# Kernel optimization log

Measured on AMD Instinct MI355X. Metric: run time of the kernel, lower is better.

## Reference

```python
import jax, jax.numpy as jnp
import numpy as np

B, S, D, H, DFF = 4, 2048, 1024, 16, 4096
HD = D // H
EPS = 1e-12

def _layernorm(x, g, b):
    mu = jnp.mean(x, axis=-1, keepdims=True)
    var = jnp.mean(jnp.square(x - mu), axis=-1, keepdims=True)
    return (x - mu) * jax.lax.rsqrt(var + EPS) * g + b

def setup_inputs() -> dict:
    key = jax.random.key(0)
    ks = jax.random.split(key, 12)
    sd = 0.02
    inp = {
        'hidden_states': jax.random.normal(ks[0], (B, S, D), jnp.float32),
        'attention_mask': jnp.zeros((B, 1, 1, S), jnp.float32),
        'Wq': jax.random.normal(ks[1], (D, D), jnp.float32) * sd,
        'bq': jnp.zeros((D,), jnp.float32),
        'Wk': jax.random.normal(ks[2], (D, D), jnp.float32) * sd,
        'bk': jnp.zeros((D,), jnp.float32),
        'Wv': jax.random.normal(ks[3], (D, D), jnp.float32) * sd,
        'bv': jnp.zeros((D,), jnp.float32),
        'Wo': jax.random.normal(ks[4], (D, D), jnp.float32) * sd,
        'bo': jnp.zeros((D,), jnp.float32),
        'ln1_g': jnp.ones((D,), jnp.float32),
        'ln1_b': jnp.zeros((D,), jnp.float32),
        'Wi': jax.random.normal(ks[5], (D, DFF), jnp.float32) * sd,
        'bi': jnp.zeros((DFF,), jnp.float32),
        'Wo2': jax.random.normal(ks[6], (DFF, D), jnp.float32) * sd,
        'bo2': jnp.zeros((D,), jnp.float32),
        'ln2_g': jnp.ones((D,), jnp.float32),
        'ln2_b': jnp.zeros((D,), jnp.float32),
    }
    return inp

def reference(hidden_states, attention_mask, Wq, bq, Wk, bk, Wv, bv, Wo, bo,
              ln1_g, ln1_b, Wi, bi, Wo2, bo2, ln2_g, ln2_b):
    x = hidden_states  # [B,S,D]
    # project and split heads -> [B,H,S,hd]
    def heads(t):
        return t.reshape(B, S, H, HD).transpose(0, 2, 1, 3)
    q = heads(x @ Wq + bq)
    k = heads(x @ Wk + bk)
    v = heads(x @ Wv + bv)
    scores = jnp.einsum('bhqd,bhkd->bhqk', q, k) / np.float32(np.sqrt(HD))
    scores = scores + attention_mask  # additive mask broadcast [B,1,1,S]
    weights = jax.nn.softmax(scores, axis=-1)
    ctx = jnp.einsum('bhqk,bhkd->bhqd', weights, v)
    ctx = ctx.transpose(0, 2, 1, 3).reshape(B, S, D)
    attn_out = _layernorm(ctx @ Wo + bo + x, ln1_g, ln1_b)
    # FFN (gelu) with residual + LayerNorm
    h = jax.nn.gelu(attn_out @ Wi + bi, approximate=False)
    out = _layernorm(h @ Wo2 + bo2 + attn_out, ln2_g, ln2_b)
    return out
```

## Files before the change

### kernel.cpp

```cpp
#include <hip/hip_runtime.h>
#include <hip/hip_bf16.h>
#include <math.h>

#define B_   4
#define S_   2048
#define D_   1024
#define H_   16
#define HD_  64
#define DFF_ 4096
#define M_   (B_*S_)

typedef __bf16 bf16x8 __attribute__((ext_vector_type(8)));
typedef __bf16 bf16x4 __attribute__((ext_vector_type(4)));
typedef float  floatx4 __attribute__((ext_vector_type(4)));

__device__ __forceinline__ float  b2f(__bf16 v) { return (float)v; }
__device__ __forceinline__ __bf16 f2b(float v)  { return (__bf16)v; }

__device__ __forceinline__ void async_ld16(const void* g, void* l) {
    __builtin_amdgcn_global_load_lds(
        (const __attribute__((address_space(1))) unsigned int*)g,
        (__attribute__((address_space(3))) unsigned int*)l, 16, 0, 0);
}

__global__ void transpose_conv_kernel(const float* __restrict__ in,
                                      __bf16* __restrict__ out, int R, int C,
                                      float scale)
{
    __shared__ float t[32][33];
    int c0 = blockIdx.x * 32, r0 = blockIdx.y * 32;
    int tx = threadIdx.x, ty = threadIdx.y;
    for (int i = ty; i < 32; i += 8)
        t[i][tx] = in[(long)(r0 + i) * C + c0 + tx];
    __syncthreads();
    for (int i = ty; i < 32; i += 8)
        out[(long)(c0 + i) * R + r0 + tx] = f2b(t[tx][i] * scale);
}

__global__ void vt_transpose_kernel(const __bf16* __restrict__ qkv,
                                    __bf16* __restrict__ vtg)
{
    __shared__ __bf16 t[32][34];
    int b  = blockIdx.z;
    int h  = blockIdx.y >> 1;
    int d0 = (blockIdx.y & 1) * 32;
    int s0 = blockIdx.x * 32;
    int tx = threadIdx.x, ty = threadIdx.y;
    for (int i = ty; i < 32; i += 8)
        t[i][tx] = qkv[(long)(b * S_ + s0 + i) * 3072 + 2048 + h * 64 + d0 + tx];
    __syncthreads();
    for (int i = ty; i < 32; i += 8)
        vtg[((long)(b * H_ + h) * 64 + d0 + i) * S_ + s0 + tx] = t[tx][i];
}

__global__ void f2b_kernel(const float* __restrict__ in, __bf16* __restrict__ out,
                           long n)
{
    long i = ((long)blockIdx.x * 256 + threadIdx.x) * 8;
    if (i >= n) return;
    float4 a = *(const float4*)&in[i];
    float4 c = *(const float4*)&in[i + 4];
    union { __bf16 h[8]; uint4 u; } p;
    p.h[0] = f2b(a.x); p.h[1] = f2b(a.y); p.h[2] = f2b(a.z); p.h[3] = f2b(a.w);
    p.h[4] = f2b(c.x); p.h[5] = f2b(c.y); p.h[6] = f2b(c.z); p.h[7] = f2b(c.w);
    *(uint4*)&out[i] = p.u;
}

__global__ void bias_concat_kernel(const float* __restrict__ bq,
                                   const float* __restrict__ bk,
                                   const float* __restrict__ bv,
                                   float* __restrict__ dst)
{
    int i = blockIdx.x * 256 + threadIdx.x;
    if (i >= 3 * D_) return;
    float v = (i < D_) ? bq[i] * 0.125f
            : (i < 2 * D_) ? bk[i - D_] : bv[i - 2 * D_];
    dst[i] = v;
}

template<int MODE>
__global__ __launch_bounds__(256, 2)
void gemm_kernel(const __bf16* __restrict__ A, const __bf16* __restrict__ Bt,
                 const float* __restrict__ bias, const float* __restrict__ resid,
                 float* __restrict__ Cf, __bf16* __restrict__ Cb,
                 int M, int N, int K)
{
    __shared__ __bf16 sA[128 * 64];
    __shared__ __bf16 sB[128 * 64];

    const int tid  = threadIdx.x;
    const int lane = tid & 63;
    const int wave = tid >> 6;
    const int wm   = (wave >> 1) * 64;
    const int wn   = (wave & 1) * 64;
    const long bm  = (long)blockIdx.y * 128;
    const long bn  = (long)blockIdx.x * 128;

    floatx4 acc[4][4];
#pragma unroll
    for (int i = 0; i < 4; ++i)
#pragma unroll
        for (int j = 0; j < 4; ++j)
#pragma unroll
            for (int r = 0; r < 4; ++r) acc[i][j][r] = 0.0f;

    const int mrow = lane & 15;
    const int quad = lane >> 4;
    const int koff0 = ((0 * 4 + quad) ^ (mrow & 7)) * 8;
    const int koff1 = ((1 * 4 + quad) ^ (mrow & 7)) * 8;

    for (int k0 = 0; k0 < K; k0 += 64) {
        __syncthreads();
#pragma unroll
        for (int t = 0; t < 4; ++t) {
            int ci  = tid + t * 256;
            int row = ci >> 3;
            int col = ((ci & 7) ^ (row & 7)) << 3;
            async_ld16(A  + (bm + row) * (long)K + k0 + col, &sA[ci * 8]);
            async_ld16(Bt + (bn + row) * (long)K + k0 + col, &sB[ci * 8]);
        }
        __syncthreads();

#pragma unroll
        for (int s = 0; s < 2; ++s) {
            const int ko = s ? koff1 : koff0;
            bf16x8 a[4], b[4];
#pragma unroll
            for (int i = 0; i < 4; ++i)
                a[i] = *(const bf16x8*)&sA[(wm + i * 16 + mrow) * 64 + ko];
#pragma unroll
            for (int j = 0; j < 4; ++j)
                b[j] = *(const bf16x8*)&sB[(wn + j * 16 + mrow) * 64 + ko];
#pragma unroll
            for (int i = 0; i < 4; ++i)
#pragma unroll
                for (int j = 0; j < 4; ++j)
                    acc[i][j] = __builtin_amdgcn_mfma_f32_16x16x32_bf16(
                        a[i], b[j], acc[i][j], 0, 0, 0);
        }
    }

    const int rq = quad * 4;
    const int cn = lane & 15;
#pragma unroll
    for (int i = 0; i < 4; ++i) {
#pragma unroll
        for (int j = 0; j < 4; ++j) {
            long col = bn + wn + j * 16 + cn;
            float bv = bias[col];
#pragma unroll
            for (int r = 0; r < 4; ++r) {
                long row = bm + wm + i * 16 + rq + r;
                float v = acc[i][j][r] + bv;
                if (MODE == 0) {
                    Cb[row * N + col] = f2b(v);
                } else if (MODE == 1) {
                    Cf[row * N + col] = v + resid[row * N + col];
                } else {
                    float g = 0.5f * v * (1.0f + erff(v * 0.70710678118654752f));
                    Cb[row * N + col] = f2b(g);
                }
            }
        }
    }
}

template<int MODE>
__global__ __launch_bounds__(512, 2)
void gemm256_kernel(const __bf16* __restrict__ A, const __bf16* __restrict__ Bt,
                    const float* __restrict__ bias, const float* __restrict__ resid,
                    float* __restrict__ Cf, __bf16* __restrict__ Cb,
                    int M, int N, int K)
{
    __shared__ __bf16 sA[2][256 * 64];
    __shared__ __bf16 sB[2][256 * 64];

    const int nbx = gridDim.x;
    const int nwg = nbx * gridDim.y;
    const int orig = blockIdx.y * nbx + blockIdx.x;
    const int q8 = nwg >> 3, r8 = nwg & 7, xcd = orig & 7, off = orig >> 3;
    const int wg = (xcd < r8 ? xcd * (q8 + 1) : r8 * (q8 + 1) + (xcd - r8) * q8) + off;
    const long bm = (long)(wg / nbx) * 256;
    const long bn = (long)(wg % nbx) * 256;

    const int tid  = threadIdx.x;
    const int lane = tid & 63;
    const int wave = tid >> 6;
    const int g    = wave >> 2;
    const int c    = wave & 3;
    const int cn   = lane & 15;
    const int quad = lane >> 4;
    const int rq   = quad * 4;

    floatx4 acc[2][2][4][2];
#pragma unroll
    for (int qi = 0; qi < 2; ++qi)
#pragma unroll
    for (int qj = 0; qj < 2; ++qj)
#pragma unroll
    for (int i = 0; i < 4; ++i)
#pragma unroll
    for (int j = 0; j < 2; ++j)
#pragma unroll
        for (int r = 0; r < 4; ++r) acc[qi][qj][i][j][r] = 0.0f;

    const int NT = K >> 6;

    auto STAGE = [&](int pb, int isB, int half, int t) {
        const __bf16* src = isB ? Bt : A;
        const long    base = isB ? bn : bm;
        __bf16*       dst  = isB ? &sB[pb][0] : &sA[pb][0];
        const int k0 = t << 6;
#pragma unroll
        for (int tt = 0; tt < 2; ++tt) {
            int ci  = tid + tt * 512;
            int row = (ci >> 3) + half * 128;
            int col = ((ci & 7) ^ (row & 7)) << 3;
            async_ld16(src + (base + row) * (long)K + k0 + col,
                       dst + half * 8192 + ci * 8);
        }
    };
    auto LDA = [&](int pb, int qi, bf16x8 (&a)[2][4]) {
#pragma unroll
        for (int i = 0; i < 4; ++i) {
            int rr = g * 64 + qi * 128 + i * 16 + cn;
#pragma unroll
            for (int s = 0; s < 2; ++s) {
                int ko = ((s * 4 + quad) ^ (rr & 7)) << 3;
                a[s][i] = *(const bf16x8*)&sA[pb][rr * 64 + ko];
            }
        }
    };
    auto LDB = [&](int pb, int qj, bf16x8 (&b)[2][2]) {
#pragma unroll
        for (int j = 0; j < 2; ++j) {
            int rr = c * 32 + qj * 128 + j * 16 + cn;
#pragma unroll
            for (int s = 0; s < 2; ++s) {
                int ko = ((s * 4 + quad) ^ (rr & 7)) << 3;
                b[s][j] = *(const bf16x8*)&sB[pb][rr * 64 + ko];
            }
        }
    };
    auto MM = [&](bf16x8 (&a)[2][4], bf16x8 (&b)[2][2], floatx4 (&ac)[4][2]) {
#pragma unroll
        for (int s = 0; s < 2; ++s)
#pragma unroll
        for (int i = 0; i < 4; ++i)
#pragma unroll
        for (int j = 0; j < 2; ++j)
            ac[i][j] = __builtin_amdgcn_mfma_f32_16x16x32_bf16(
                a[s][i], b[s][j], ac[i][j], 0, 0, 0);
    };

    STAGE(0, 0, 0, 0); STAGE(0, 1, 0, 0); STAGE(0, 1, 1, 0); STAGE(0, 0, 1, 0);
    STAGE(1, 0, 0, 1); STAGE(1, 1, 1, 1);
    asm volatile("s_waitcnt vmcnt(4)" ::: "memory");
    __builtin_amdgcn_s_barrier();
    __builtin_amdgcn_sched_barrier(0);

    bf16x8 a[2][4], b[2][2];
    for (int t = 0; t < NT; ++t) {
        const int pb = t & 1;
        LDA(pb, 0, a); LDB(pb, 0, b);
        if (t + 1 < NT) STAGE(pb ^ 1, 0, 1, t + 1);
        asm volatile("s_waitcnt lgkmcnt(8)" ::: "memory");
        __builtin_amdgcn_s_barrier();
        asm volatile("s_waitcnt lgkmcnt(0)" ::: "memory");
        __builtin_amdgcn_sched_barrier(0);
        __builtin_amdgcn_s_setprio(1);
        MM(a, b, acc[0][0]);
        __builtin_amdgcn_s_setprio(0);
        __builtin_amdgcn_s_barrier();
        __builtin_amdgcn_sched_barrier(0);
        LDB(pb, 1, b);
        if (t + 1 < NT) STAGE(pb ^ 1, 1, 0, t + 1);
        __builtin_amdgcn_s_barrier();
        asm volatile("s_waitcnt lgkmcnt(0)" ::: "memory");
        __builtin_amdgcn_sched_barrier(0);
        __builtin_amdgcn_s_setprio(1);
        MM(a, b, acc[0][1]);
        __builtin_amdgcn_s_setprio(0);
        __builtin_amdgcn_s_barrier();
        __builtin_amdgcn_sched_barrier(0);
        LDA(pb, 1, a);
        if (t + 2 < NT) STAGE(pb, 0, 0, t + 2);
        __builtin_amdgcn_s_barrier();
        asm volatile("s_waitcnt lgkmcnt(0)" ::: "memory");
        __builtin_amdgcn_sched_barrier(0);
        __builtin_amdgcn_s_setprio(1);
        MM(a, b, acc[1][1]);
        __builtin_amdgcn_s_setprio(0);
        __builtin_amdgcn_s_barrier();
        __builtin_amdgcn_sched_barrier(0);
        LDB(pb, 0, b);
        if (t + 2 < NT) STAGE(pb, 1, 1, t + 2);
        if (t + 1 < NT) {
            asm volatile("s_waitcnt vmcnt(4)" ::: "memory");
        } else {
            asm volatile("s_waitcnt vmcnt(0)" ::: "memory");
        }
        __builtin_amdgcn_s_barrier();
        asm volatile("s_waitcnt lgkmcnt(0)" ::: "memory");
        __builtin_amdgcn_sched_barrier(0);
        __builtin_amdgcn_s_setprio(1);
        MM(a, b, acc[1][0]);
        __builtin_amdgcn_s_setprio(0);
        __builtin_amdgcn_s_barrier();
        __builtin_amdgcn_sched_barrier(0);
    }

#pragma unroll
    for (int qi = 0; qi < 2; ++qi)
#pragma unroll
    for (int i = 0; i < 4; ++i)
#pragma unroll
    for (int qj = 0; qj < 2; ++qj)
#pragma unroll
    for (int j = 0; j < 2; ++j) {
        long col = bn + c * 32 + qj * 128 + j * 16 + cn;
        float bv = bias[col];
#pragma unroll
        for (int r = 0; r < 4; ++r) {
            long row = bm + g * 64 + qi * 128 + i * 16 + rq + r;
            float v = acc[qi][qj][i][j][r] + bv;
            if (MODE == 0) {
                Cb[row * N + col] = f2b(v);
            } else if (MODE == 1) {
                Cf[row * N + col] = v + resid[row * N + col];
            } else {
                float ge = 0.5f * v * (1.0f + erff(v * 0.70710678118654752f));
                Cb[row * N + col] = f2b(ge);
            }
        }
    }
}

__global__ __launch_bounds__(256, 2)
void attn_kernel(const __bf16* __restrict__ QKV, const __bf16* __restrict__ VT,
                 const float* __restrict__ mask, __bf16* __restrict__ ctx)
{
    __shared__ __bf16 Qs[64 * 64];
    __shared__ __bf16 Ks[64 * 64];
    __shared__ __bf16 Vt[64 * 64];
    __shared__ __bf16 Ps[64 * 64];

    const int tid  = threadIdx.x;
    const int lane = tid & 63;
    const int wave = tid >> 6;
    const int w16  = wave * 16;
    const int b    = blockIdx.z, h = blockIdx.y;
    const int q0   = blockIdx.x * 64;
    const int cn   = lane & 15;
    const int quad = lane >> 4;
    const int rq   = quad * 4;
    const int koff0 = ((0 * 4 + quad) ^ (cn & 7)) * 8;
    const int koff1 = ((1 * 4 + quad) ^ (cn & 7)) * 8;

#pragma unroll
    for (int t = 0; t < 2; ++t) {
        int ci = tid + t * 256;
        int qr = ci >> 3, dc = ((ci & 7) ^ (qr & 7)) << 3;
        async_ld16(QKV + (long)(b * S_ + q0 + qr) * 3072 + h * 64 + dc,
                   &Qs[ci * 8]);
    }
    __syncthreads();
    const bf16x8 aq0 = *(const bf16x8*)&Qs[(w16 + cn) * 64 + koff0];
    const bf16x8 aq1 = *(const bf16x8*)&Qs[(w16 + cn) * 64 + koff1];

    float l_[4];
    floatx4 o_[4];
#pragma unroll
    for (int r = 0; r < 4; ++r) l_[r] = 0.0f;
#pragma unroll
    for (int jt = 0; jt < 4; ++jt)
#pragma unroll
        for (int r = 0; r < 4; ++r) o_[jt][r] = 0.0f;

    const long vbase = ((long)(b * H_ + h) * 64) * S_;

    for (int k0 = 0; k0 < S_; k0 += 64) {
        __syncthreads();
#pragma unroll
        for (int t = 0; t < 2; ++t) {
            int ci = tid + t * 256;
            int kr = ci >> 3, dc = ((ci & 7) ^ (kr & 7)) << 3;
            async_ld16(QKV + (long)(b * S_ + k0 + kr) * 3072 + 1024 + h * 64 + dc,
                       &Ks[ci * 8]);
            int vd = ci >> 3, kc = ((ci & 7) ^ (vd & 7)) << 3;
            async_ld16(VT + vbase + (long)vd * S_ + k0 + kc, &Vt[ci * 8]);
        }
        __syncthreads();

        floatx4 st[4];
#pragma unroll
        for (int jt = 0; jt < 4; ++jt)
#pragma unroll
            for (int r = 0; r < 4; ++r) st[jt][r] = 0.0f;
#pragma unroll
        for (int jt = 0; jt < 4; ++jt) {
            bf16x8 b0 = *(const bf16x8*)&Ks[(jt * 16 + cn) * 64 + koff0];
            bf16x8 b1 = *(const bf16x8*)&Ks[(jt * 16 + cn) * 64 + koff1];
            st[jt] = __builtin_amdgcn_mfma_f32_16x16x32_bf16(aq0, b0, st[jt], 0, 0, 0);
            st[jt] = __builtin_amdgcn_mfma_f32_16x16x32_bf16(aq1, b1, st[jt], 0, 0, 0);
        }
#pragma unroll
        for (int jt = 0; jt < 4; ++jt) {
            float mv = mask[(long)b * S_ + k0 + jt * 16 + cn] - 8.0f;
#pragma unroll
            for (int r = 0; r < 4; ++r) {
                float p = __expf(st[jt][r] + mv);
                st[jt][r] = p;
                l_[r] += p;
            }
        }
#pragma unroll
        for (int jt = 0; jt < 4; ++jt)
#pragma unroll
            for (int r = 0; r < 4; ++r) {
                int prow = w16 + rq + r;
                int pcol = (((jt * 2 + (cn >> 3)) ^ (prow & 7)) << 3) + (cn & 7);
                Ps[prow * 64 + pcol] = f2b(st[jt][r]);
            }

        {
            bf16x8 ap0 = *(const bf16x8*)&Ps[(w16 + cn) * 64 + koff0];
            bf16x8 ap1 = *(const bf16x8*)&Ps[(w16 + cn) * 64 + koff1];
#pragma unroll
            for (int jt = 0; jt < 4; ++jt) {
                bf16x8 b0 = *(const bf16x8*)&Vt[(jt * 16 + cn) * 64 + koff0];
                bf16x8 b1 = *(const bf16x8*)&Vt[(jt * 16 + cn) * 64 + koff1];
                o_[jt] = __builtin_amdgcn_mfma_f32_16x16x32_bf16(ap0, b0, o_[jt], 0, 0, 0);
                o_[jt] = __builtin_amdgcn_mfma_f32_16x16x32_bf16(ap1, b1, o_[jt], 0, 0, 0);
            }
        }
    }

#pragma unroll
    for (int r = 0; r < 4; ++r) {
        float l = l_[r];
        l += __shfl_xor(l, 1);
        l += __shfl_xor(l, 2);
        l += __shfl_xor(l, 4);
        l += __shfl_xor(l, 8);
        float linv = 1.0f / l;
        long rowg = (long)(b * S_ + q0 + w16 + rq + r) * D_ + h * 64;
#pragma unroll
        for (int jt = 0; jt < 4; ++jt)
            ctx[rowg + jt * 16 + cn] = f2b(o_[jt][r] * linv);
    }
}

__global__ __launch_bounds__(256)
void ln_kernel(const float* __restrict__ X, const float* __restrict__ gamma,
               const float* __restrict__ beta, float* __restrict__ out,
               __bf16* __restrict__ outb)
{
    const long row = blockIdx.x;
    const int tid = threadIdx.x;
    const float* x = X + row * D_;
    float4 v = *(const float4*)&x[tid * 4];
    float s  = v.x + v.y + v.z + v.w;
    float s2 = v.x * v.x + v.y * v.y + v.z * v.z + v.w * v.w;
    for (int off = 32; off > 0; off >>= 1) {
        s  += __shfl_down(s, off);
        s2 += __shfl_down(s2, off);
    }
    __shared__ float red[8];
    int wave = tid >> 6, lane = tid & 63;
    if (lane == 0) { red[wave] = s; red[4 + wave] = s2; }
    __syncthreads();
    float ts  = red[0] + red[1] + red[2] + red[3];
    float ts2 = red[4] + red[5] + red[6] + red[7];
    float mu  = ts * (1.0f / D_);
    float var = ts2 * (1.0f / D_) - mu * mu;
    float rs  = rsqrtf(fmaxf(var, 0.0f) + 1e-12f);
    float4 g = *(const float4*)&gamma[tid * 4];
    float4 b = *(const float4*)&beta[tid * 4];
    float4 o;
    o.x = (v.x - mu) * rs * g.x + b.x;
    o.y = (v.y - mu) * rs * g.y + b.y;
    o.z = (v.z - mu) * rs * g.z + b.z;
    o.w = (v.w - mu) * rs * g.w + b.w;
    *(float4*)&out[row * D_ + tid * 4] = o;
    if (outb) {
        bf16x4 ob;
        ob[0] = f2b(o.x); ob[1] = f2b(o.y); ob[2] = f2b(o.z); ob[3] = f2b(o.w);
        *(bf16x4*)&outb[row * D_ + tid * 4] = ob;
    }
}

extern "C" void kernel_launch(void* const* d_in, const int* in_sizes, int n_in,
                              void* d_out, int out_size, void* d_ws, size_t ws_size,
                              hipStream_t stream)
{
    const float* hid  = (const float*)d_in[0];
    const float* mask = (const float*)d_in[1];
    const float* Wq   = (const float*)d_in[2];
    const float* bq   = (const float*)d_in[3];
    const float* Wk   = (const float*)d_in[4];
    const float* bk   = (const float*)d_in[5];
    const float* Wv   = (const float*)d_in[6];
    const float* bv   = (const float*)d_in[7];
    const float* Wo   = (const float*)d_in[8];
    const float* bo   = (const float*)d_in[9];
    const float* g1   = (const float*)d_in[10];
    const float* b1   = (const float*)d_in[11];
    const float* Wi   = (const float*)d_in[12];
    const float* bi   = (const float*)d_in[13];
    const float* Wo2  = (const float*)d_in[14];
    const float* bo2  = (const float*)d_in[15];
    const float* g2   = (const float*)d_in[16];
    const float* b2   = (const float*)d_in[17];
    float* out = (float*)d_out;

    char* w = (char*)d_ws;
    auto take = [&](size_t bytes) { char* p = w; w += bytes; return p; };
    __bf16* wqkvb = (__bf16*)take((size_t)3 * D_ * D_ * 2);
    __bf16* wob   = (__bf16*)take((size_t)D_ * D_ * 2);
    __bf16* wib   = (__bf16*)take((size_t)D_ * DFF_ * 2);
    __bf16* wo2b  = (__bf16*)take((size_t)D_ * DFF_ * 2);
    float*  qkvbias = (float*)take(16384);
    __bf16* qkv   = (__bf16*)take((size_t)M_ * 3 * D_ * 2);
    __bf16* ctxb  = (__bf16*)take((size_t)M_ * D_ * 2);
    __bf16* hb    = (__bf16*)take((size_t)M_ * D_ * 2);
    float*  tmp      = (float*)take((size_t)M_ * D_ * 4);
    float*  attn_out = (float*)take((size_t)M_ * D_ * 4);
    __bf16* hbuf = qkv;
    __bf16* vtg  = hb;
    __bf16* attn_out_b = hb;
    (void)in_sizes; (void)n_in; (void)out_size; (void)ws_size;

    dim3 tb(32, 8);
    transpose_conv_kernel<<<dim3(D_/32, D_/32), tb, 0, stream>>>(Wq, wqkvb,            D_, D_, 0.125f);
    transpose_conv_kernel<<<dim3(D_/32, D_/32), tb, 0, stream>>>(Wk, wqkvb + D_*D_,    D_, D_, 1.0f);
    transpose_conv_kernel<<<dim3(D_/32, D_/32), tb, 0, stream>>>(Wv, wqkvb + 2*D_*D_,  D_, D_, 1.0f);
    transpose_conv_kernel<<<dim3(D_/32, D_/32), tb, 0, stream>>>(Wo, wob, D_, D_, 1.0f);
    transpose_conv_kernel<<<dim3(DFF_/32, D_/32), tb, 0, stream>>>(Wi, wib, D_, DFF_, 1.0f);
    transpose_conv_kernel<<<dim3(D_/32, DFF_/32), tb, 0, stream>>>(Wo2, wo2b, DFF_, D_, 1.0f);
    bias_concat_kernel<<<12, 256, 0, stream>>>(bq, bk, bv, qkvbias);
    f2b_kernel<<<(M_*D_/8 + 255)/256, 256, 0, stream>>>(hid, hb, (long)M_*D_);

    gemm256_kernel<0><<<dim3(3*D_/256, M_/256), 512, 0, stream>>>(
        hb, wqkvb, qkvbias, nullptr, nullptr, qkv, M_, 3*D_, D_);

    vt_transpose_kernel<<<dim3(S_/32, H_*2, B_), tb, 0, stream>>>(qkv, vtg);

    attn_kernel<<<dim3(S_/64, H_, B_), 256, 0, stream>>>(qkv, vtg, mask, ctxb);

    gemm_kernel<1><<<dim3(D_/128, M_/128), 256, 0, stream>>>(
        ctxb, wob, bo, hid, tmp, nullptr, M_, D_, D_);
    ln_kernel<<<M_, 256, 0, stream>>>(tmp, g1, b1, attn_out, attn_out_b);

    gemm256_kernel<2><<<dim3(DFF_/256, M_/256), 512, 0, stream>>>(
        attn_out_b, wib, bi, nullptr, nullptr, hbuf, M_, DFF_, D_);
    gemm_kernel<1><<<dim3(D_/128, M_/128), 256, 0, stream>>>(
        hbuf, wo2b, bo2, attn_out, tmp, nullptr, M_, D_, DFF_);
    ln_kernel<<<M_, 256, 0, stream>>>(tmp, g2, b2, out, nullptr);
}
```

Measured before the change: 622.8 us.

## Double-buffer K/V tiles in attention and prefetch next tile during compute

The attention kernel now keeps two shared-memory buffers for K and V and issues async loads for the next key tile before computing on the current one, replacing the two __syncthreads per iteration with a single waitcnt plus barrier at the end. Mask values are also prefetched one tile ahead, Q is staged through the P buffer to save LDS, and s_setprio is raised around the MFMA blocks. This is meant to hide global-load latency behind the matmuls. The cost is extra LDS per block, which may reduce occupancy, and reuse of the Ps buffer for Q depends on correct barrier ordering.

```diff
diff --git a/kernel.cpp b/kernel.cpp
--- a/kernel.cpp
+++ b/kernel.cpp
@@ -340,9 +340,8 @@
 void attn_kernel(const __bf16* __restrict__ QKV, const __bf16* __restrict__ VT,
                  const float* __restrict__ mask, __bf16* __restrict__ ctx)
 {
-    __shared__ __bf16 Qs[64 * 64];
-    __shared__ __bf16 Ks[64 * 64];
-    __shared__ __bf16 Vt[64 * 64];
+    __shared__ __bf16 Ks[2][64 * 64];
+    __shared__ __bf16 Vt[2][64 * 64];
     __shared__ __bf16 Ps[64 * 64];
 
     const int tid  = threadIdx.x;
@@ -357,16 +356,38 @@
     const int koff0 = ((0 * 4 + quad) ^ (cn & 7)) * 8;
     const int koff1 = ((1 * 4 + quad) ^ (cn & 7)) * 8;
 
+    const long vbase = ((long)(b * H_ + h) * 64) * S_;
+
+    auto STAGE = [&](int bufi, int k0) {
+#pragma unroll
+        for (int t = 0; t < 2; ++t) {
+            int ci = tid + t * 256;
+            int r  = ci >> 3;
+            int cz = ((ci & 7) ^ (r & 7)) << 3;
+            async_ld16(QKV + (long)(b * S_ + k0 + r) * 3072 + 1024 + h * 64 + cz,
+                       &Ks[bufi][ci * 8]);
+            async_ld16(VT + vbase + (long)r * S_ + k0 + cz, &Vt[bufi][ci * 8]);
+        }
+    };
+
 #pragma unroll
     for (int t = 0; t < 2; ++t) {
         int ci = tid + t * 256;
         int qr = ci >> 3, dc = ((ci & 7) ^ (qr & 7)) << 3;
         async_ld16(QKV + (long)(b * S_ + q0 + qr) * 3072 + h * 64 + dc,
-                   &Qs[ci * 8]);
-    }
-    __syncthreads();
-    const bf16x8 aq0 = *(const bf16x8*)&Qs[(w16 + cn) * 64 + koff0];
-    const bf16x8 aq1 = *(const bf16x8*)&Qs[(w16 + cn) * 64 + koff1];
+                   &Ps[ci * 8]);
+    }
+    STAGE(0, 0);
+    float mv[4];
+#pragma unroll
+    for (int jt = 0; jt < 4; ++jt)
+        mv[jt] = mask[(long)b * S_ + jt * 16 + cn] - 8.0f;
+    asm volatile("s_waitcnt vmcnt(0)" ::: "memory");
+    __builtin_amdgcn_s_barrier();
+    __builtin_amdgcn_sched_barrier(0);
+
+    const bf16x8 aq0 = *(const bf16x8*)&Ps[(w16 + cn) * 64 + koff0];
+    const bf16x8 aq1 = *(const bf16x8*)&Ps[(w16 + cn) * 64 + koff1];
 
     float l_[4];
     floatx4 o_[4];
@@ -377,39 +398,35 @@
 #pragma unroll
         for (int r = 0; r < 4; ++r) o_[jt][r] = 0.0f;
 
-    const long vbase = ((long)(b * H_ + h) * 64) * S_;
-
+    int cur = 0;
     for (int k0 = 0; k0 < S_; k0 += 64) {
-        __syncthreads();
-#pragma unroll
-        for (int t = 0; t < 2; ++t) {
-            int ci = tid + t * 256;
-            int kr = ci >> 3, dc = ((ci & 7) ^ (kr & 7)) << 3;
-            async_ld16(QKV + (long)(b * S_ + k0 + kr) * 3072 + 1024 + h * 64 + dc,
-                       &Ks[ci * 8]);
-            int vd = ci >> 3, kc = ((ci & 7) ^ (vd & 7)) << 3;
-            async_ld16(VT + vbase + (long)vd * S_ + k0 + kc, &Vt[ci * 8]);
-        }
-        __syncthreads();
+        float mvn[4];
+        if (k0 + 64 < S_) {
+            STAGE(cur ^ 1, k0 + 64);
+#pragma unroll
+            for (int jt = 0; jt < 4; ++jt)
+                mvn[jt] = mask[(long)b * S_ + k0 + 64 + jt * 16 + cn] - 8.0f;
+        }
 
         floatx4 st[4];
 #pragma unroll
         for (int jt = 0; jt < 4; ++jt)
 #pragma unroll
             for (int r = 0; r < 4; ++r) st[jt][r] = 0.0f;
+        __builtin_amdgcn_s_setprio(1);
 #pragma unroll
         for (int jt = 0; jt < 4; ++jt) {
-            bf16x8 b0 = *(const bf16x8*)&Ks[(jt * 16 + cn) * 64 + koff0];
-            bf16x8 b1 = *(const bf16x8*)&Ks[(jt * 16 + cn) * 64 + koff1];
+            bf16x8 b0 = *(const bf16x8*)&Ks[cur][(jt * 16 + cn) * 64 + koff0];
+            bf16x8 b1 = *(const bf16x8*)&Ks[cur][(jt * 16 + cn) * 64 + koff1];
             st[jt] = __builtin_amdgcn_mfma_f32_16x16x32_bf16(aq0, b0, st[jt], 0, 0, 0);
             st[jt] = __builtin_amdgcn_mfma_f32_16x16x32_bf16(aq1, b1, st[jt], 0, 0, 0);
         }
+        __builtin_amdgcn_s_setprio(0);
 #pragma unroll
         for (int jt = 0; jt < 4; ++jt) {
-            float mv = mask[(long)b * S_ + k0 + jt * 16 + cn] - 8.0f;
 #pragma unroll
             for (int r = 0; r < 4; ++r) {
-                float p = __expf(st[jt][r] + mv);
+                float p = __expf(st[jt][r] + mv[jt]);
                 st[jt][r] = p;
                 l_[r] += p;
             }
@@ -426,14 +443,25 @@
         {
             bf16x8 ap0 = *(const bf16x8*)&Ps[(w16 + cn) * 64 + koff0];
             bf16x8 ap1 = *(const bf16x8*)&Ps[(w16 + cn) * 64 + koff1];
+            __builtin_amdgcn_s_setprio(1);
 #pragma unroll
             for (int jt = 0; jt < 4; ++jt) {
-                bf16x8 b0 = *(const bf16x8*)&Vt[(jt * 16 + cn) * 64 + koff0];
-                bf16x8 b1 = *(const bf16x8*)&Vt[(jt * 16 + cn) * 64 + koff1];
+                bf16x8 b0 = *(const bf16x8*)&Vt[cur][(jt * 16 + cn) * 64 + koff0];
+                bf16x8 b1 = *(const bf16x8*)&Vt[cur][(jt * 16 + cn) * 64 + koff1];
                 o_[jt] = __builtin_amdgcn_mfma_f32_16x16x32_bf16(ap0, b0, o_[jt], 0, 0, 0);
                 o_[jt] = __builtin_amdgcn_mfma_f32_16x16x32_bf16(ap1, b1, o_[jt], 0, 0, 0);
             }
-        }
+            __builtin_amdgcn_s_setprio(0);
+        }
+
+        asm volatile("s_waitcnt vmcnt(0) lgkmcnt(0)" ::: "memory");
+        __builtin_amdgcn_s_barrier();
+        __builtin_amdgcn_sched_barrier(0);
+        if (k0 + 64 < S_) {
+#pragma unroll
+            for (int jt = 0; jt < 4; ++jt) mv[jt] = mvn[jt];
+        }
+        cur ^= 1;
     }
 
 #pragma unroll
```

After: 601.3 us. 1.04x faster.
